# Kernel optimization log

Hardware: AMD Instinct MI355X
Metric: run time of the kernel (lower is better)

Reference implementation:

```python
import jax, jax.numpy as jnp
import numpy as np

# Vim-S config
B, L, D, DEPTH = 16, 197, 384, 24
DI, DS, DTR = 768, 16, 24  # d_inner=2*D, d_state, dt_rank=ceil(D/16)
NUM_CLASSES = 1000
EPS = 1e-5


def setup_inputs() -> dict:
    key = jax.random.key(0)
    ks = jax.random.split(key, 12)
    f = jnp.float32
    rn = lambda k, shp, s=0.02: jax.random.normal(k, shp, f) * s
    inp = {
        'x': jax.random.normal(ks[0], (B, 3, 224, 224), f),
        'patch_w': rn(ks[1], (D, 3, 16, 16)),
        'patch_b': jnp.zeros((D,), f),
        'cls_token': rn(ks[2], (1, 1, D)),
        'pos_embed': rn(ks[3], (1, L, D)),
        'in_proj_w': rn(ks[4], (DEPTH, 2 * DI, D)),
        'conv_w': rn(ks[5], (DEPTH, DI, 1, 4), 0.1),  # depthwise causal conv, d_conv=4
        'conv_b': jnp.zeros((DEPTH, DI), f),
        'x_proj_w': rn(ks[6], (DEPTH, DTR + 2 * DS, DI)),
        'dt_proj_w': rn(ks[7], (DEPTH, DI, DTR), 0.1),
        'dt_proj_b': jnp.full((DEPTH, DI), float(np.log(np.expm1(0.01))), f),
        'A_log': jnp.log(jnp.broadcast_to(jnp.arange(1, DS + 1, dtype=f), (DEPTH, DI, DS))),
        'D_ssm': jnp.ones((DEPTH, DI), f),
        'out_proj_w': rn(ks[8], (DEPTH, D, DI)),
        'norm_w': jnp.ones((DEPTH, D), f),
        'norm_b': jnp.zeros((DEPTH, D), f),
        'normf_w': jnp.ones((D,), f),
        'normf_b': jnp.zeros((D,), f),
        'head_w': rn(ks[9], (NUM_CLASSES, D)),
        'head_b': jnp.zeros((NUM_CLASSES,), f),
    }
    return inp


def _ln(u, w, b):
    mu = u.mean(-1, keepdims=True)
    v = ((u - mu) ** 2).mean(-1, keepdims=True)
    return (u - mu) * jax.lax.rsqrt(v + EPS) * w + b


def _silu(u):
    return u * jax.nn.sigmoid(u)


def _mixer(u, Win, Wc, bc, Wx, Wdt, bdt, Alog, Dp, Wout):
    # u: [B, L, D]
    xz = jnp.einsum('bld,ed->ble', u, Win)            # [B, L, 2*DI]
    xc, z = jnp.split(xz, 2, axis=-1)
    # causal depthwise conv1d (d_conv=4): pad 3 on the left
    xt = jnp.pad(xc.transpose(0, 2, 1), ((0, 0), (0, 0), (3, 0)))
    xt = jax.lax.conv_general_dilated(xt, Wc, (1,), 'VALID',
                                      dimension_numbers=('NCH', 'OIH', 'NCH'),
                                      feature_group_count=DI)
    xc = _silu((xt + bc[None, :, None]).transpose(0, 2, 1))  # [B, L, DI]
    dbl = jnp.einsum('bld,ed->ble', xc, Wx)           # [B, L, DTR+2*DS]
    dt = jax.nn.softplus(jnp.einsum('blr,dr->bld', dbl[..., :DTR], Wdt) + bdt)
    Bm = dbl[..., DTR:DTR + DS]                       # [B, L, DS]
    Cm = dbl[..., DTR + DS:]                          # [B, L, DS]
    A = -jnp.exp(Alog)                                # [DI, DS]
    dA = jnp.exp(jnp.einsum('bld,dn->bldn', dt, A))   # [B, L, DI, DS]
    dBx = jnp.einsum('bld,bln->bldn', dt * xc, Bm)    # [B, L, DI, DS]

    def step(h, inps):
        dA_t, dBx_t, C_t = inps
        h = dA_t * h + dBx_t                          # [B, DI, DS]
        return h, jnp.einsum('bdn,bn->bd', h, C_t)

    h0 = jnp.zeros((u.shape[0], DI, DS), u.dtype)
    _, ys = jax.lax.scan(step, h0, (dA.transpose(1, 0, 2, 3),
                                    dBx.transpose(1, 0, 2, 3),
                                    Cm.transpose(1, 0, 2)))
    y = ys.transpose(1, 0, 2) + xc * Dp               # [B, L, DI]
    y = y * _silu(z)
    return jnp.einsum('ble,de->bld', y, Wout)         # [B, L, D]


def reference(x, patch_w, patch_b, cls_token, pos_embed, in_proj_w, conv_w, conv_b,
              x_proj_w, dt_proj_w, dt_proj_b, A_log, D_ssm, out_proj_w,
              norm_w, norm_b, normf_w, normf_b, head_w, head_b):
    b = x.shape[0]
    # patch embed: Conv2d(3, D, 16, stride 16)
    feat = jax.lax.conv_general_dilated(x, patch_w, (16, 16), 'VALID',
                                        dimension_numbers=('NCHW', 'OIHW', 'NCHW'))
    feat = feat + patch_b[None, :, None, None]
    tokens = feat.reshape(b, D, -1).transpose(0, 2, 1)          # [B, 196, D]
    h = jnp.concatenate([jnp.broadcast_to(cls_token, (b, 1, D)), tokens], axis=1)
    h = h + pos_embed                                           # [B, 197, D]

    def layer(carry, p):
        hid, res = carry
        Win, Wc, bc, Wx, Wdt, bdt, Alog, Dp, Wout, nw, nb = p
        res = res + hid                # (hidden + residual), first layer: residual = hidden
        hid = _mixer(_ln(res, nw, nb), Win, Wc, bc, Wx, Wdt, bdt, Alog, Dp, Wout)
        return (hid, res), None

    (hid, res), _ = jax.lax.scan(layer, (h, jnp.zeros_like(h)),
                                 (in_proj_w, conv_w, conv_b, x_proj_w, dt_proj_w,
                                  dt_proj_b, A_log, D_ssm, out_proj_w, norm_w, norm_b))
    out = _ln(res + hid, normf_w, normf_b)
    return out[:, 0] @ head_w.T + head_b                        # [B, num_classes]
```

## Files before the change

### kernel.cpp

```cpp
#include <hip/hip_runtime.h>
#include <hip/hip_bf16.h>
#include <math.h>

#define BB     16
#define LL     197
#define DD     384
#define DEPTH  24
#define DI     768
#define DSN    16
#define DTR    24
#define NC     1000
#define TT     (BB*LL)
#define NPATCH 196
#define EPSV   1e-5f

#define NCHUNK 12
#define CH     17

typedef __attribute__((ext_vector_type(8))) short short8;
typedef __attribute__((ext_vector_type(4))) short short4v;
typedef __attribute__((ext_vector_type(4))) float f32x4;

__device__ __forceinline__ short f2bf(float f) {
  union { float f; unsigned u; } v; v.f = f;
  unsigned u = v.u + 0x7fffu + ((v.u >> 16) & 1u);
  return (short)(u >> 16);
}

__device__ __forceinline__ void gload16(const short* g, const short* l) {
  __builtin_amdgcn_global_load_lds(
      (const __attribute__((address_space(1))) unsigned int*)g,
      (__attribute__((address_space(3))) unsigned int*)l, 16, 0, 0);
}

__global__ __launch_bounds__(256) void k_cvt(const float* __restrict__ src,
                                             short* __restrict__ dst, int n) {
  int i = (blockIdx.x * 256 + threadIdx.x) * 4;
  if (i + 3 < n) {
    float4 v = *(const float4*)&src[i];
    short4v o = {f2bf(v.x), f2bf(v.y), f2bf(v.z), f2bf(v.w)};
    *(short4v*)&dst[i] = o;
  } else {
    for (int j = 0; i + j < n && j < 4; j++) dst[i + j] = f2bf(src[i + j]);
  }
}

__global__ __launch_bounds__(256) void k_init(const float* __restrict__ cls,
                                              const float* __restrict__ pos,
                                              float* __restrict__ res,
                                              float* __restrict__ hid) {
  int i = blockIdx.x * 256 + threadIdx.x;
  if (i < TT * DD) res[i] = 0.f;
  if (i < BB * DD) {
    int b = i / DD, d = i % DD;
    hid[(size_t)(b * LL) * DD + d] = cls[d] + pos[d];
  }
}

__global__ __launch_bounds__(256) void k_patch(const float* __restrict__ x,
                                               const float* __restrict__ pw,
                                               const float* __restrict__ pb,
                                               const float* __restrict__ pos,
                                               float* __restrict__ hid) {
  __shared__ short sA[64 * 40];
  __shared__ short sB[64 * 40];
  const int tid = threadIdx.x;
  const int m0 = blockIdx.x * 64, n0 = blockIdx.y * 64;
  const int srow = tid >> 2;
  const int skq = (tid & 3) * 8;
  const int lane = tid & 63, w = tid >> 6;
  const int wm = (w >> 1) * 32, wn = (w & 1) * 32;
  const int fr = lane & 15;
  const int fk = (lane >> 4) * 8;
  f32x4 acc[2][2] = {};
  const int m = m0 + srow;
  const int b = m / NPATCH;
  const int p = m % NPATCH;
  const int ph = p / 14, pwi = p % 14;
  const float* Wrow = pw + (size_t)(n0 + srow) * 768 + skq;
  for (int k0 = 0; k0 < 768; k0 += 32) {
    int k = k0 + skq;
    int c = k >> 8, rr = (k >> 4) & 15, kw = k & 15;
    const float* xrow = &x[(size_t)(((b * 3 + c) * 224) + (ph * 16 + rr)) * 224 +
                           (pwi * 16 + kw)];
    float4 a0 = *(const float4*)&xrow[0];
    float4 a1 = *(const float4*)&xrow[4];
    float4 b0 = *(const float4*)&Wrow[k0];
    float4 b1 = *(const float4*)&Wrow[k0 + 4];
    short8 av = {f2bf(a0.x), f2bf(a0.y), f2bf(a0.z), f2bf(a0.w),
                 f2bf(a1.x), f2bf(a1.y), f2bf(a1.z), f2bf(a1.w)};
    short8 bv = {f2bf(b0.x), f2bf(b0.y), f2bf(b0.z), f2bf(b0.w),
                 f2bf(b1.x), f2bf(b1.y), f2bf(b1.z), f2bf(b1.w)};
    *(short8*)&sA[srow * 40 + skq] = av;
    *(short8*)&sB[srow * 40 + skq] = bv;
    __syncthreads();
    short8 af0 = *(const short8*)&sA[(wm + fr) * 40 + fk];
    short8 af1 = *(const short8*)&sA[(wm + 16 + fr) * 40 + fk];
    short8 bf0 = *(const short8*)&sB[(wn + fr) * 40 + fk];
    short8 bf1 = *(const short8*)&sB[(wn + 16 + fr) * 40 + fk];
    acc[0][0] = __builtin_amdgcn_mfma_f32_16x16x32_bf16(af0, bf0, acc[0][0], 0, 0, 0);
    acc[0][1] = __builtin_amdgcn_mfma_f32_16x16x32_bf16(af0, bf1, acc[0][1], 0, 0, 0);
    acc[1][0] = __builtin_amdgcn_mfma_f32_16x16x32_bf16(af1, bf0, acc[1][0], 0, 0, 0);
    acc[1][1] = __builtin_amdgcn_mfma_f32_16x16x32_bf16(af1, bf1, acc[1][1], 0, 0, 0);
    __syncthreads();
  }
#pragma unroll
  for (int i = 0; i < 2; i++)
#pragma unroll
    for (int j = 0; j < 2; j++)
#pragma unroll
      for (int q = 0; q < 4; q++) {
        int mm = m0 + wm + i * 16 + (lane >> 4) * 4 + q;
        int nn = n0 + wn + j * 16 + (lane & 15);
        int b2 = mm / NPATCH, pp = mm % NPATCH;
        int tok = b2 * LL + 1 + pp;
        hid[(size_t)tok * DD + nn] = acc[i][j][q] + pb[nn] + pos[(size_t)(1 + pp) * DD + nn];
      }
}

__global__ __launch_bounds__(256) void k_gemm128(const short* __restrict__ A, int lda,
                                                 const short* __restrict__ W, int ldb,
                                                 float* __restrict__ C, int ldc,
                                                 int M, int N, int K) {
  __shared__ short sA[128 * 32];
  __shared__ short sB[128 * 32];
  const int tid = threadIdx.x;
  const int lane = tid & 63, w = tid >> 6;
  const int m0 = blockIdx.x * 128, n0 = blockIdx.y * 128;
  const int wm = (w >> 1) * 64, wn = (w & 1) * 64;
  const int fr = lane & 15;
  const int fk = (lane >> 4) * 8;
  const int q0 = w * 2, q1 = w * 2 + 1;
  const int sr0 = q0 * 16 + (lane >> 2);
  const int sr1 = q1 * 16 + (lane >> 2);
  const int scol = (lane & 3) * 8;
  f32x4 acc[4][4] = {};
  const short* Ab0 = A + (size_t)(m0 + sr0) * lda + scol;
  const short* Ab1 = A + (size_t)(m0 + sr1) * lda + scol;
  const short* Bb0 = W + (size_t)(n0 + sr0) * ldb + scol;
  const short* Bb1 = W + (size_t)(n0 + sr1) * ldb + scol;
  for (int k0 = 0; k0 < K; k0 += 32) {
    gload16(Ab0 + k0, &sA[q0 * 512]);
    gload16(Ab1 + k0, &sA[q1 * 512]);
    gload16(Bb0 + k0, &sB[q0 * 512]);
    gload16(Bb1 + k0, &sB[q1 * 512]);
    __syncthreads();
    short8 af[4], bf[4];
#pragma unroll
    for (int i = 0; i < 4; i++) {
      af[i] = *(const short8*)&sA[(wm + i * 16 + fr) * 32 + fk];
      bf[i] = *(const short8*)&sB[(wn + i * 16 + fr) * 32 + fk];
    }
#pragma unroll
    for (int i = 0; i < 4; i++)
#pragma unroll
      for (int j = 0; j < 4; j++)
        acc[i][j] = __builtin_amdgcn_mfma_f32_16x16x32_bf16(af[i], bf[j], acc[i][j], 0, 0, 0);
    __syncthreads();
  }
#pragma unroll
  for (int i = 0; i < 4; i++)
#pragma unroll
    for (int j = 0; j < 4; j++)
#pragma unroll
      for (int q = 0; q < 4; q++) {
        int mm = m0 + wm + i * 16 + (lane >> 4) * 4 + q;
        int nn = n0 + wn + j * 16 + fr;
        if (mm < M) C[(size_t)mm * ldc + nn] = acc[i][j][q];
      }
}

__global__ __launch_bounds__(256) void k_gemm64(const short* __restrict__ A, int lda,
                                                const short* __restrict__ W, int ldb,
                                                float* __restrict__ C, int ldc,
                                                int M, int N, int K) {
  __shared__ short sA[64 * 32];
  __shared__ short sB[64 * 32];
  const int tid = threadIdx.x;
  const int lane = tid & 63, w = tid >> 6;
  const int m0 = blockIdx.x * 64, n0 = blockIdx.y * 64;
  const int wm = (w >> 1) * 32, wn = (w & 1) * 32;
  const int fr = lane & 15;
  const int fk = (lane >> 4) * 8;
  const int srow = w * 16 + (lane >> 2);
  const int scol = (lane & 3) * 8;
  f32x4 acc[2][2] = {};
  const short* Ab = A + (size_t)(m0 + srow) * lda + scol;
  const short* Bb = W + (size_t)(n0 + srow) * ldb + scol;
  for (int k0 = 0; k0 < K; k0 += 32) {
    gload16(Ab + k0, &sA[w * 512]);
    gload16(Bb + k0, &sB[w * 512]);
    __syncthreads();
    short8 af0 = *(const short8*)&sA[(wm + fr) * 32 + fk];
    short8 af1 = *(const short8*)&sA[(wm + 16 + fr) * 32 + fk];
    short8 bf0 = *(const short8*)&sB[(wn + fr) * 32 + fk];
    short8 bf1 = *(const short8*)&sB[(wn + 16 + fr) * 32 + fk];
    acc[0][0] = __builtin_amdgcn_mfma_f32_16x16x32_bf16(af0, bf0, acc[0][0], 0, 0, 0);
    acc[0][1] = __builtin_amdgcn_mfma_f32_16x16x32_bf16(af0, bf1, acc[0][1], 0, 0, 0);
    acc[1][0] = __builtin_amdgcn_mfma_f32_16x16x32_bf16(af1, bf0, acc[1][0], 0, 0, 0);
    acc[1][1] = __builtin_amdgcn_mfma_f32_16x16x32_bf16(af1, bf1, acc[1][1], 0, 0, 0);
    __syncthreads();
  }
#pragma unroll
  for (int i = 0; i < 2; i++)
#pragma unroll
    for (int j = 0; j < 2; j++)
#pragma unroll
      for (int q = 0; q < 4; q++) {
        int mm = m0 + wm + i * 16 + (lane >> 4) * 4 + q;
        int nn = n0 + wn + j * 16 + fr;
        if (mm < M) C[(size_t)mm * ldc + nn] = acc[i][j][q];
      }
}

__global__ __launch_bounds__(256) void k_cxd(const float* __restrict__ xz,
                                             const float* __restrict__ wc,
                                             const float* __restrict__ bc,
                                             const short* __restrict__ wx,
                                             const short* __restrict__ wdt,
                                             const float* __restrict__ dbias,
                                             float* __restrict__ xc,
                                             float* __restrict__ dbl,
                                             float* __restrict__ dtb) {
  __shared__ short sXC[16 * 776];
  __shared__ short sB[4 * 64 * 32];
  __shared__ short sDT[16 * 40];
  const int tid = threadIdx.x;
  const int t0 = blockIdx.x * 16;
  for (int it = 0; it < 12; it++) {
    int g = tid + it * 256;
    int tl = g / 192, eg = g % 192;
    int e = eg * 4;
    int t = t0 + tl;
    int b = t / LL, l = t % LL;
    const float* base = xz + (size_t)(b * LL) * (2 * DI) + e;
    float4 w0 = *(const float4*)&wc[(e + 0) * 4];
    float4 w1 = *(const float4*)&wc[(e + 1) * 4];
    float4 w2 = *(const float4*)&wc[(e + 2) * 4];
    float4 w3 = *(const float4*)&wc[(e + 3) * 4];
    float4 acc = *(const float4*)&bc[e];
    if (l >= 3) {
      float4 xv = *(const float4*)&base[(size_t)(l - 3) * (2 * DI)];
      acc.x += xv.x * w0.x; acc.y += xv.y * w1.x; acc.z += xv.z * w2.x; acc.w += xv.w * w3.x;
    }
    if (l >= 2) {
      float4 xv = *(const float4*)&base[(size_t)(l - 2) * (2 * DI)];
      acc.x += xv.x * w0.y; acc.y += xv.y * w1.y; acc.z += xv.z * w2.y; acc.w += xv.w * w3.y;
    }
    if (l >= 1) {
      float4 xv = *(const float4*)&base[(size_t)(l - 1) * (2 * DI)];
      acc.x += xv.x * w0.z; acc.y += xv.y * w1.z; acc.z += xv.z * w2.z; acc.w += xv.w * w3.z;
    }
    {
      float4 xv = *(const float4*)&base[(size_t)l * (2 * DI)];
      acc.x += xv.x * w0.w; acc.y += xv.y * w1.w; acc.z += xv.z * w2.w; acc.w += xv.w * w3.w;
    }
    acc.x = acc.x / (1.f + __expf(-acc.x));
    acc.y = acc.y / (1.f + __expf(-acc.y));
    acc.z = acc.z / (1.f + __expf(-acc.z));
    acc.w = acc.w / (1.f + __expf(-acc.w));
    *(float4*)&xc[(size_t)t * DI + e] = acc;
    short4v ov = {f2bf(acc.x), f2bf(acc.y), f2bf(acc.z), f2bf(acc.w)};
    *(short4v*)&sXC[tl * 776 + e] = ov;
  }
  __syncthreads();
  const int lane = tid & 63, w = tid >> 6;
  const int fr = lane & 15;
  const int fk = (lane >> 4) * 8;
  const int srow = w * 16 + (lane >> 2);
  const int scol = (lane & 3) * 8;
  const short* Bb = wx + (size_t)srow * DI + scol;
  f32x4 accx = {};
  for (int kc = 0; kc < DI; kc += 128) {
#pragma unroll
    for (int s = 0; s < 4; s++)
      gload16(Bb + kc + s * 32, &sB[s * 2048 + w * 512]);
    __syncthreads();
#pragma unroll
    for (int s = 0; s < 4; s++) {
      short8 af = *(const short8*)&sXC[fr * 776 + kc + s * 32 + fk];
      short8 bf = *(const short8*)&sB[s * 2048 + (w * 16 + fr) * 32 + fk];
      accx = __builtin_amdgcn_mfma_f32_16x16x32_bf16(af, bf, accx, 0, 0, 0);
    }
    __syncthreads();
  }
  {
    int nn = w * 16 + (lane & 15);
#pragma unroll
    for (int q = 0; q < 4; q++) {
      int row = (lane >> 4) * 4 + q;
      int t = t0 + row;
      if (nn >= DTR && nn < 56) dbl[(size_t)t * 56 + nn] = accx[q];
      if (w < 2) sDT[row * 40 + nn] = (nn < DTR) ? f2bf(accx[q]) : (short)0;
    }
  }
  __syncthreads();
  short8 adt = *(const short8*)&sDT[fr * 40 + fk];
  const int g = lane >> 4;
  for (int jj = 0; jj < 12; jj++) {
    int j = w * 12 + jj;
    int row = j * 16 + fr;
    short8 bdt = {0, 0, 0, 0, 0, 0, 0, 0};
    if (g < 3) bdt = *(const short8*)&wdt[(size_t)row * DTR + g * 8];
    f32x4 p = {};
    p = __builtin_amdgcn_mfma_f32_16x16x32_bf16(adt, bdt, p, 0, 0, 0);
    int nn = j * 16 + (lane & 15);
    float bv = dbias[nn];
#pragma unroll
    for (int q = 0; q < 4; q++) {
      int t = t0 + (lane >> 4) * 4 + q;
      float v = p[q] + bv;
      v = (v > 20.f) ? v : log1pf(__expf(v));
      dtb[(size_t)t * DI + nn] = v;
    }
  }
}

__global__ __launch_bounds__(256) void k_scan1(const float* __restrict__ dt,
                                               const float* __restrict__ xc,
                                               const float* __restrict__ dbl,
                                               const float* __restrict__ Alog,
                                               float* __restrict__ Aprod,
                                               float* __restrict__ Hend) {
  const int tid = threadIdx.x;
  const int e = blockIdx.x * 128 + (tid >> 1);
  const int nh = tid & 1;
  const int b = blockIdx.y;
  const int c = blockIdx.z;
  float4 al0 = *(const float4*)&Alog[(size_t)e * DSN + nh * 8];
  float4 al1 = *(const float4*)&Alog[(size_t)e * DSN + nh * 8 + 4];
  float negA[8] = {-__expf(al0.x), -__expf(al0.y), -__expf(al0.z), -__expf(al0.w),
                   -__expf(al1.x), -__expf(al1.y), -__expf(al1.z), -__expf(al1.w)};
  float h[8] = {};
  float asum = 0.f;
  const int l0 = c * CH;
  const int l1 = (l0 + CH < LL) ? (l0 + CH) : LL;
  const size_t tbase = (size_t)b * LL;
  for (int l = l0; l < l1; l++) {
    size_t t = tbase + l;
    float dtv = dt[t * DI + e];
    float xcv = xc[t * DI + e];
    float4 B0 = *(const float4*)&dbl[t * 56 + DTR + nh * 8];
    float4 B1 = *(const float4*)&dbl[t * 56 + DTR + nh * 8 + 4];
    float dx = dtv * xcv;
    float Bv[8] = {B0.x, B0.y, B0.z, B0.w, B1.x, B1.y, B1.z, B1.w};
#pragma unroll
    for (int j = 0; j < 8; j++)
      h[j] = __expf(dtv * negA[j]) * h[j] + dx * Bv[j];
    asum += dtv;
  }
  size_t ci = (((size_t)c * BB + b) * DI + e) * DSN + nh * 8;
  *(float4*)&Aprod[ci] = float4{__expf(asum * negA[0]), __expf(asum * negA[1]),
                                __expf(asum * negA[2]), __expf(asum * negA[3])};
  *(float4*)&Aprod[ci + 4] = float4{__expf(asum * negA[4]), __expf(asum * negA[5]),
                                    __expf(asum * negA[6]), __expf(asum * negA[7])};
  *(float4*)&Hend[ci] = float4{h[0], h[1], h[2], h[3]};
  *(float4*)&Hend[ci + 4] = float4{h[4], h[5], h[6], h[7]};
}

__global__ __launch_bounds__(256) void k_scan2(const float* __restrict__ dt,
                                               const float* __restrict__ xc,
                                               const float* __restrict__ xz,
                                               const float* __restrict__ dbl,
                                               const float* __restrict__ Alog,
                                               const float* __restrict__ Dp,
                                               const float* __restrict__ Aprod,
                                               const float* __restrict__ Hend,
                                               short* __restrict__ ybf) {
  const int tid = threadIdx.x;
  const int e = blockIdx.x * 128 + (tid >> 1);
  const int nh = tid & 1;
  const int b = blockIdx.y;
  const int c = blockIdx.z;
  float4 al0 = *(const float4*)&Alog[(size_t)e * DSN + nh * 8];
  float4 al1 = *(const float4*)&Alog[(size_t)e * DSN + nh * 8 + 4];
  float negA[8] = {-__expf(al0.x), -__expf(al0.y), -__expf(al0.z), -__expf(al0.w),
                   -__expf(al1.x), -__expf(al1.y), -__expf(al1.z), -__expf(al1.w)};
  const float dpv = Dp[e];
  float h[8] = {};
  const size_t cstride = (size_t)BB * DI * DSN;
  const size_t cbase = (((size_t)b * DI + e) * DSN) + nh * 8;
  for (int cp = 0; cp < c; cp++) {
    size_t ci = (size_t)cp * cstride + cbase;
    float4 a0 = *(const float4*)&Aprod[ci];
    float4 a1 = *(const float4*)&Aprod[ci + 4];
    float4 e0 = *(const float4*)&Hend[ci];
    float4 e1 = *(const float4*)&Hend[ci + 4];
    h[0] = a0.x * h[0] + e0.x; h[1] = a0.y * h[1] + e0.y;
    h[2] = a0.z * h[2] + e0.z; h[3] = a0.w * h[3] + e0.w;
    h[4] = a1.x * h[4] + e1.x; h[5] = a1.y * h[5] + e1.y;
    h[6] = a1.z * h[6] + e1.z; h[7] = a1.w * h[7] + e1.w;
  }
  const int l0 = c * CH;
  const int l1 = (l0 + CH < LL) ? (l0 + CH) : LL;
  const size_t tbase = (size_t)b * LL;
  for (int l = l0; l < l1; l++) {
    size_t t = tbase + l;
    float dtv = dt[t * DI + e];
    float xcv = xc[t * DI + e];
    float zv = xz[t * (2 * DI) + DI + e];
    float4 B0 = *(const float4*)&dbl[t * 56 + DTR + nh * 8];
    float4 B1 = *(const float4*)&dbl[t * 56 + DTR + nh * 8 + 4];
    float4 C0 = *(const float4*)&dbl[t * 56 + DTR + DSN + nh * 8];
    float4 C1 = *(const float4*)&dbl[t * 56 + DTR + DSN + nh * 8 + 4];
    float dx = dtv * xcv;
    float Bv[8] = {B0.x, B0.y, B0.z, B0.w, B1.x, B1.y, B1.z, B1.w};
    float Cv[8] = {C0.x, C0.y, C0.z, C0.w, C1.x, C1.y, C1.z, C1.w};
    float acc = 0.f;
#pragma unroll
    for (int j = 0; j < 8; j++) {
      h[j] = __expf(dtv * negA[j]) * h[j] + dx * Bv[j];
      acc += h[j] * Cv[j];
    }
    acc += __shfl_xor(acc, 1);
    if (nh == 0) {
      float sz = zv * (1.f / (1.f + __expf(-zv)));
      ybf[t * DI + e] = f2bf((acc + xcv * dpv) * sz);
    }
  }
}

__global__ __launch_bounds__(256) void k_addln(float* __restrict__ res,
                                               const float* __restrict__ hid,
                                               short* __restrict__ u,
                                               const float* __restrict__ nw,
                                               const float* __restrict__ nb) {
  const int lane = threadIdx.x & 63;
  const int t = blockIdx.x * 4 + (threadIdx.x >> 6);
  float r[6];
  float s = 0.f, sq = 0.f;
#pragma unroll
  for (int j = 0; j < 6; j++) {
    int d = lane + j * 64;
    float v = res[(size_t)t * DD + d] + hid[(size_t)t * DD + d];
    res[(size_t)t * DD + d] = v;
    r[j] = v;
    s += v; sq += v * v;
  }
#pragma unroll
  for (int o = 32; o > 0; o >>= 1) { s += __shfl_xor(s, o); sq += __shfl_xor(sq, o); }
  float mu = s * (1.f / 384.f);
  float var = sq * (1.f / 384.f) - mu * mu;
  float rs = rsqrtf(var + EPSV);
#pragma unroll
  for (int j = 0; j < 6; j++) {
    int d = lane + j * 64;
    u[(size_t)t * DD + d] = f2bf((r[j] - mu) * rs * nw[d] + nb[d]);
  }
}

__global__ __launch_bounds__(256) void k_final(const float* __restrict__ res,
                                               const float* __restrict__ hid,
                                               const float* __restrict__ nfw,
                                               const float* __restrict__ nfb,
                                               const float* __restrict__ hw,
                                               const float* __restrict__ hb,
                                               float* __restrict__ out) {
  const int b = blockIdx.y;
  const int c0 = blockIdx.x * 125;
  const int tid = threadIdx.x;
  __shared__ float u0[DD];
  __shared__ float ls[4], lq[4];
  const size_t t0 = (size_t)b * LL * DD;
  float v0 = res[t0 + tid] + hid[t0 + tid];
  float v1 = (tid < 128) ? (res[t0 + 256 + tid] + hid[t0 + 256 + tid]) : 0.f;
  float s = v0 + v1, sq = v0 * v0 + v1 * v1;
#pragma unroll
  for (int o = 32; o > 0; o >>= 1) { s += __shfl_xor(s, o); sq += __shfl_xor(sq, o); }
  if ((tid & 63) == 0) { ls[tid >> 6] = s; lq[tid >> 6] = sq; }
  __syncthreads();
  float st = ls[0] + ls[1] + ls[2] + ls[3];
  float qt = lq[0] + lq[1] + lq[2] + lq[3];
  float mu = st * (1.f / 384.f);
  float var = qt * (1.f / 384.f) - mu * mu;
  float rs = rsqrtf(var + EPSV);
  u0[tid] = (v0 - mu) * rs * nfw[tid] + nfb[tid];
  if (tid < 128) u0[256 + tid] = (v1 - mu) * rs * nfw[256 + tid] + nfb[256 + tid];
  __syncthreads();
  int c = c0 + tid;
  if (tid < 125 && c < NC) {
    float acc = hb[c];
    const float* wrow = hw + (size_t)c * DD;
    for (int d = 0; d < DD; d += 4) {
      float4 w4 = *(const float4*)&wrow[d];
      acc += u0[d] * w4.x + u0[d + 1] * w4.y + u0[d + 2] * w4.z + u0[d + 3] * w4.w;
    }
    out[(size_t)b * NC + c] = acc;
  }
}

extern "C" void kernel_launch(void* const* d_in, const int* in_sizes, int n_in,
                              void* d_out, int out_size, void* d_ws, size_t ws_size,
                              hipStream_t stream) {
  const float* x       = (const float*)d_in[0];
  const float* patch_w = (const float*)d_in[1];
  const float* patch_b = (const float*)d_in[2];
  const float* cls     = (const float*)d_in[3];
  const float* pos     = (const float*)d_in[4];
  const float* in_proj = (const float*)d_in[5];
  const float* conv_w  = (const float*)d_in[6];
  const float* conv_b  = (const float*)d_in[7];
  const float* x_proj  = (const float*)d_in[8];
  const float* dt_w    = (const float*)d_in[9];
  const float* dt_b    = (const float*)d_in[10];
  const float* A_log   = (const float*)d_in[11];
  const float* D_ssm   = (const float*)d_in[12];
  const float* out_w   = (const float*)d_in[13];
  const float* norm_w  = (const float*)d_in[14];
  const float* norm_b  = (const float*)d_in[15];
  const float* normf_w = (const float*)d_in[16];
  const float* normf_b = (const float*)d_in[17];
  const float* head_w  = (const float*)d_in[18];
  const float* head_b  = (const float*)d_in[19];
  float* out = (float*)d_out;

  float* ws = (float*)d_ws;
  float* res = ws;  ws += (size_t)TT * DD;
  float* hid = ws;  ws += (size_t)TT * DD;
  float* u_r = ws;  ws += (size_t)TT * DD;
  float* xzb = ws;  ws += (size_t)TT * 2 * DI;
  float* xcb = ws;  ws += (size_t)TT * DI;
  float* dbl = ws;  ws += (size_t)TT * 56;
  float* dtb = ws;  ws += (size_t)TT * DI;
  float* ybf_r = ws; ws += (size_t)TT * DI / 2;
  float* Aprod = ws; ws += (size_t)NCHUNK * BB * DI * DSN;
  float* Hend  = ws; ws += (size_t)NCHUNK * BB * DI * DSN;
  short* winbf  = (short*)ws; ws += (size_t)DEPTH * 2 * DI * DD / 2;
  short* woutbf = (short*)ws; ws += (size_t)DEPTH * DD * DI / 2;
  short* wxbf   = (short*)ws; ws += (size_t)DEPTH * 56 * DI / 2;
  short* wdtbf  = (short*)ws; ws += (size_t)DEPTH * DI * DTR / 2;

  short* u    = (short*)u_r;
  short* ybf  = (short*)ybf_r;

  {
    int n1 = DEPTH * 2 * DI * DD;
    k_cvt<<<(n1 / 4 + 255) / 256, 256, 0, stream>>>(in_proj, winbf, n1);
    int n2 = DEPTH * DD * DI;
    k_cvt<<<(n2 / 4 + 255) / 256, 256, 0, stream>>>(out_w, woutbf, n2);
    int n3 = DEPTH * 56 * DI;
    k_cvt<<<(n3 / 4 + 255) / 256, 256, 0, stream>>>(x_proj, wxbf, n3);
    int n4 = DEPTH * DI * DTR;
    k_cvt<<<(n4 / 4 + 255) / 256, 256, 0, stream>>>(dt_w, wdtbf, n4);
  }

  k_init<<<(TT * DD + 255) / 256, 256, 0, stream>>>(cls, pos, res, hid);
  k_patch<<<dim3(49, 6), 256, 0, stream>>>(x, patch_w, patch_b, pos, hid);

  for (int layer = 0; layer < DEPTH; layer++) {
    k_addln<<<TT / 4, 256, 0, stream>>>(res, hid, u, norm_w + layer * DD,
                                        norm_b + layer * DD);
    k_gemm128<<<dim3(25, 12), 256, 0, stream>>>(
        u, DD, winbf + (size_t)layer * 2 * DI * DD, DD, xzb, 2 * DI, TT, 2 * DI, DD);
    k_cxd<<<dim3(TT / 16), 256, 0, stream>>>(
        xzb, conv_w + layer * DI * 4, conv_b + layer * DI,
        wxbf + (size_t)layer * 56 * DI, wdtbf + (size_t)layer * DI * DTR,
        dt_b + layer * DI, xcb, dbl, dtb);
    k_scan1<<<dim3(DI / 128, BB, NCHUNK - 1), 256, 0, stream>>>(
        dtb, xcb, dbl, A_log + (size_t)layer * DI * DSN, Aprod, Hend);
    k_scan2<<<dim3(DI / 128, BB, NCHUNK), 256, 0, stream>>>(
        dtb, xcb, xzb, dbl, A_log + (size_t)layer * DI * DSN,
        D_ssm + layer * DI, Aprod, Hend, ybf);
    k_gemm64<<<dim3(50, 6), 256, 0, stream>>>(
        ybf, DI, woutbf + (size_t)layer * DD * DI, DI, hid, DD, TT, DD, DI);
  }

  k_final<<<dim3(8, BB), 256, 0, stream>>>(res, hid, normf_w, normf_b, head_w, head_b, out);
}
```

Before: 2.869 ms.

## Split conv+xproj kernel into elementwise conv and direct-load x_proj/dt kernels

Splits the fused conv/x_proj/dt_proj kernel into two launches. The first is a flat elementwise causal conv + SiLU that writes both an fp32 and a bf16 copy of xc to global memory. The second loads its MFMA operands straight from global memory with no LDS staging or barriers, unrolls the dt loop, and swaps log1pf for the faster __logf(1+exp) softplus. It removes the large shared-memory footprint and the syncs, which should raise occupancy, at the cost of an extra global round trip for bf16 xc, one more launch per layer, and slightly lower softplus accuracy.

```diff
diff --git a/kernel.cpp b/kernel.cpp
--- a/kernel.cpp
+++ b/kernel.cpp
@@ -213,79 +213,71 @@
       }
 }
 
-__global__ __launch_bounds__(256) void k_cxd(const float* __restrict__ xz,
-                                             const float* __restrict__ wc,
-                                             const float* __restrict__ bc,
-                                             const short* __restrict__ wx,
-                                             const short* __restrict__ wdt,
-                                             const float* __restrict__ dbias,
-                                             float* __restrict__ xc,
-                                             float* __restrict__ dbl,
-                                             float* __restrict__ dtb) {
-  __shared__ short sXC[16 * 776];
-  __shared__ short sB[4 * 64 * 32];
+__global__ __launch_bounds__(256) void k_conv(const float* __restrict__ xz,
+                                              const float* __restrict__ wc,
+                                              const float* __restrict__ bc,
+                                              float* __restrict__ xc,
+                                              short* __restrict__ xcbf) {
+  int i = blockIdx.x * 256 + threadIdx.x;
+  if (i >= TT * (DI / 4)) return;
+  int eg = i % (DI / 4);
+  int t = i / (DI / 4);
+  int e = eg * 4;
+  int b = t / LL, l = t % LL;
+  const float* base = xz + (size_t)(b * LL) * (2 * DI) + e;
+  float4 w0 = *(const float4*)&wc[(e + 0) * 4];
+  float4 w1 = *(const float4*)&wc[(e + 1) * 4];
+  float4 w2 = *(const float4*)&wc[(e + 2) * 4];
+  float4 w3 = *(const float4*)&wc[(e + 3) * 4];
+  float4 acc = *(const float4*)&bc[e];
+  if (l >= 3) {
+    float4 xv = *(const float4*)&base[(size_t)(l - 3) * (2 * DI)];
+    acc.x += xv.x * w0.x; acc.y += xv.y * w1.x; acc.z += xv.z * w2.x; acc.w += xv.w * w3.x;
+  }
+  if (l >= 2) {
+    float4 xv = *(const float4*)&base[(size_t)(l - 2) * (2 * DI)];
+    acc.x += xv.x * w0.y; acc.y += xv.y * w1.y; acc.z += xv.z * w2.y; acc.w += xv.w * w3.y;
+  }
+  if (l >= 1) {
+    float4 xv = *(const float4*)&base[(size_t)(l - 1) * (2 * DI)];
+    acc.x += xv.x * w0.z; acc.y += xv.y * w1.z; acc.z += xv.z * w2.z; acc.w += xv.w * w3.z;
+  }
+  {
+    float4 xv = *(const float4*)&base[(size_t)l * (2 * DI)];
+    acc.x += xv.x * w0.w; acc.y += xv.y * w1.w; acc.z += xv.z * w2.w; acc.w += xv.w * w3.w;
+  }
+  acc.x = acc.x / (1.f + __expf(-acc.x));
+  acc.y = acc.y / (1.f + __expf(-acc.y));
+  acc.z = acc.z / (1.f + __expf(-acc.z));
+  acc.w = acc.w / (1.f + __expf(-acc.w));
+  *(float4*)&xc[(size_t)t * DI + e] = acc;
+  short4v ov = {f2bf(acc.x), f2bf(acc.y), f2bf(acc.z), f2bf(acc.w)};
+  *(short4v*)&xcbf[(size_t)t * DI + e] = ov;
+}
+
+__global__ __launch_bounds__(256) void k_xd(const short* __restrict__ xcbf,
+                                            const short* __restrict__ wx,
+                                            const short* __restrict__ wdt,
+                                            const float* __restrict__ dbias,
+                                            float* __restrict__ dbl,
+                                            float* __restrict__ dtb) {
   __shared__ short sDT[16 * 40];
   const int tid = threadIdx.x;
   const int t0 = blockIdx.x * 16;
-  for (int it = 0; it < 12; it++) {
-    int g = tid + it * 256;
-    int tl = g / 192, eg = g % 192;
-    int e = eg * 4;
-    int t = t0 + tl;
-    int b = t / LL, l = t % LL;
-    const float* base = xz + (size_t)(b * LL) * (2 * DI) + e;
-    float4 w0 = *(const float4*)&wc[(e + 0) * 4];
-    float4 w1 = *(const float4*)&wc[(e + 1) * 4];
-    float4 w2 = *(const float4*)&wc[(e + 2) * 4];
-    float4 w3 = *(const float4*)&wc[(e + 3) * 4];
-    float4 acc = *(const float4*)&bc[e];
-    if (l >= 3) {
-      float4 xv = *(const float4*)&base[(size_t)(l - 3) * (2 * DI)];
-      acc.x += xv.x * w0.x; acc.y += xv.y * w1.x; acc.z += xv.z * w2.x; acc.w += xv.w * w3.x;
-    }
-    if (l >= 2) {
-      float4 xv = *(const float4*)&base[(size_t)(l - 2) * (2 * DI)];
-      acc.x += xv.x * w0.y; acc.y += xv.y * w1.y; acc.z += xv.z * w2.y; acc.w += xv.w * w3.y;
-    }
-    if (l >= 1) {
-      float4 xv = *(const float4*)&base[(size_t)(l - 1) * (2 * DI)];
-      acc.x += xv.x * w0.z; acc.y += xv.y * w1.z; acc.z += xv.z * w2.z; acc.w += xv.w * w3.z;
-    }
-    {
-      float4 xv = *(const float4*)&base[(size_t)l * (2 * DI)];
-      acc.x += xv.x * w0.w; acc.y += xv.y * w1.w; acc.z += xv.z * w2.w; acc.w += xv.w * w3.w;
-    }
-    acc.x = acc.x / (1.f + __expf(-acc.x));
-    acc.y = acc.y / (1.f + __expf(-acc.y));
-    acc.z = acc.z / (1.f + __expf(-acc.z));
-    acc.w = acc.w / (1.f + __expf(-acc.w));
-    *(float4*)&xc[(size_t)t * DI + e] = acc;
-    short4v ov = {f2bf(acc.x), f2bf(acc.y), f2bf(acc.z), f2bf(acc.w)};
-    *(short4v*)&sXC[tl * 776 + e] = ov;
-  }
-  __syncthreads();
   const int lane = tid & 63, w = tid >> 6;
   const int fr = lane & 15;
   const int fk = (lane >> 4) * 8;
-  const int srow = w * 16 + (lane >> 2);
-  const int scol = (lane & 3) * 8;
-  const short* Bb = wx + (size_t)srow * DI + scol;
   f32x4 accx = {};
-  for (int kc = 0; kc < DI; kc += 128) {
-#pragma unroll
-    for (int s = 0; s < 4; s++)
-      gload16(Bb + kc + s * 32, &sB[s * 2048 + w * 512]);
-    __syncthreads();
-#pragma unroll
-    for (int s = 0; s < 4; s++) {
-      short8 af = *(const short8*)&sXC[fr * 776 + kc + s * 32 + fk];
-      short8 bf = *(const short8*)&sB[s * 2048 + (w * 16 + fr) * 32 + fk];
-      accx = __builtin_amdgcn_mfma_f32_16x16x32_bf16(af, bf, accx, 0, 0, 0);
-    }
-    __syncthreads();
+  const short* Arow = xcbf + (size_t)(t0 + fr) * DI + fk;
+  const short* Wrow = wx + (size_t)(w * 16 + fr) * DI + fk;
+#pragma unroll
+  for (int k0 = 0; k0 < DI; k0 += 32) {
+    short8 af = *(const short8*)&Arow[k0];
+    short8 bf = *(const short8*)&Wrow[k0];
+    accx = __builtin_amdgcn_mfma_f32_16x16x32_bf16(af, bf, accx, 0, 0, 0);
   }
   {
-    int nn = w * 16 + (lane & 15);
+    int nn = w * 16 + fr;
 #pragma unroll
     for (int q = 0; q < 4; q++) {
       int row = (lane >> 4) * 4 + q;
@@ -297,21 +289,21 @@
   __syncthreads();
   short8 adt = *(const short8*)&sDT[fr * 40 + fk];
   const int g = lane >> 4;
+#pragma unroll
   for (int jj = 0; jj < 12; jj++) {
     int j = w * 12 + jj;
-    int row = j * 16 + fr;
-    short8 bdt = {0, 0, 0, 0, 0, 0, 0, 0};
-    if (g < 3) bdt = *(const short8*)&wdt[(size_t)row * DTR + g * 8];
+    short8 bdt = short8{0, 0, 0, 0, 0, 0, 0, 0};
+    if (g < 3) bdt = *(const short8*)&wdt[(size_t)(j * 16 + fr) * DTR + g * 8];
     f32x4 p = {};
     p = __builtin_amdgcn_mfma_f32_16x16x32_bf16(adt, bdt, p, 0, 0, 0);
-    int nn = j * 16 + (lane & 15);
-    float bv = dbias[nn];
+    int nc = j * 16 + fr;
+    float bv = dbias[nc];
 #pragma unroll
     for (int q = 0; q < 4; q++) {
       int t = t0 + (lane >> 4) * 4 + q;
       float v = p[q] + bv;
-      v = (v > 20.f) ? v : log1pf(__expf(v));
-      dtb[(size_t)t * DI + nn] = v;
+      v = (v > 20.f) ? v : __logf(1.f + __expf(v));
+      dtb[(size_t)t * DI + nc] = v;
     }
   }
 }
@@ -523,6 +515,7 @@
   float* dbl = ws;  ws += (size_t)TT * 56;
   float* dtb = ws;  ws += (size_t)TT * DI;
   float* ybf_r = ws; ws += (size_t)TT * DI / 2;
+  float* xcbf_r = ws; ws += (size_t)TT * DI / 2;
   float* Aprod = ws; ws += (size_t)NCHUNK * BB * DI * DSN;
   float* Hend  = ws; ws += (size_t)NCHUNK * BB * DI * DSN;
   short* winbf  = (short*)ws; ws += (size_t)DEPTH * 2 * DI * DD / 2;
@@ -532,6 +525,7 @@
 
   short* u    = (short*)u_r;
   short* ybf  = (short*)ybf_r;
+  short* xcbf = (short*)xcbf_r;
 
   {
     int n1 = DEPTH * 2 * DI * DD;
@@ -552,10 +546,11 @@
                                         norm_b + layer * DD);
     k_gemm128<<<dim3(25, 12), 256, 0, stream>>>(
         u, DD, winbf + (size_t)layer * 2 * DI * DD, DD, xzb, 2 * DI, TT, 2 * DI, DD);
-    k_cxd<<<dim3(TT / 16), 256, 0, stream>>>(
-        xzb, conv_w + layer * DI * 4, conv_b + layer * DI,
-        wxbf + (size_t)layer * 56 * DI, wdtbf + (size_t)layer * DI * DTR,
-        dt_b + layer * DI, xcb, dbl, dtb);
+    k_conv<<<(TT * (DI / 4) + 255) / 256, 256, 0, stream>>>(
+        xzb, conv_w + layer * DI * 4, conv_b + layer * DI, xcb, xcbf);
+    k_xd<<<dim3(TT / 16), 256, 0, stream>>>(
+        xcbf, wxbf + (size_t)layer * 56 * DI, wdtbf + (size_t)layer * DI * DTR,
+        dt_b + layer * DI, dbl, dtb);
     k_scan1<<<dim3(DI / 128, BB, NCHUNK - 1), 256, 0, stream>>>(
         dtb, xcb, dbl, A_log + (size_t)layer * DI * DSN, Aprod, Hend);
     k_scan2<<<dim3(DI / 128, BB, NCHUNK), 256, 0, stream>>>(
```

After: 2.594 ms. -9.6%, faster.
